# Kernel tuning notes

Hardware: AMD Instinct MI355X
Metric: run time of the kernel (lower is better)

The kernel has to match this reference:

```python
import jax, jax.numpy as jnp
import numpy as np

B, N, F, L = 4, 8192, 64, 2


def setup_inputs() -> dict:
    key = jax.random.key(0)
    k1, k2, k3 = jax.random.split(key, 3)
    x = jax.random.normal(k1, (B, N, F), dtype=jnp.float32)
    net_params = jax.random.normal(k2, (L * F * F,), dtype=jnp.float32)
    A = jax.random.normal(k3, (N, N), dtype=jnp.float32)
    return {"x": x, "t": 0, "net_params": net_params, "A": A}


def reference(x, t, net_params, A):
    # weights: [L, F, F]
    weights = net_params.reshape(L, F, F)
    # x: [B, N, F] (original does x.view(-1, A.size(1), features))
    z = x.reshape(-1, A.shape[1], F)
    for i in range(L):
        # GCN_operation: Z_out = A @ Z @ W_i  (the nested vmm loops emulate exactly this)
        h = jnp.einsum('mn,bnf->bmf', A, z)          # [B, N, F]
        z = jnp.einsum('bmf,fg->bmg', h, weights[i])  # [B, N, F]
        z = jax.nn.relu(z)
    return z
```

## Files before the change

kernel.cpp:

```cpp
#include <hip/hip_runtime.h>
#include <stdint.h>


#define MK 8192

typedef float f32x4 __attribute__((ext_vector_type(4)));
typedef uint32_t u32x4 __attribute__((ext_vector_type(4)));
typedef uint32_t u32x2 __attribute__((ext_vector_type(2)));
typedef __bf16 bf16x8 __attribute__((ext_vector_type(8)));

__device__ inline uint16_t f2bf(float f) {
  uint32_t u = __builtin_bit_cast(uint32_t, f);
  u += 0x7fffu + ((u >> 16) & 1u);
  return (uint16_t)(u >> 16);
}
__device__ inline float bf2f(uint32_t lo16) {
  return __builtin_bit_cast(float, lo16 << 16);
}

#define GLD(src, dstbase)                                                                    \
  __builtin_amdgcn_global_load_lds((const __attribute__((address_space(1))) uint32_t*)(src), \
                                   (__attribute__((address_space(3))) uint32_t*)(dstbase),   \
                                   16, 0, 0)

__global__ __launch_bounds__(256) void zw0(const float* __restrict__ x,
                                           const float* __restrict__ net,
                                           uint16_t* __restrict__ Zt) {
  __shared__ float Wl[64 * 64];
  __shared__ float rows[64][65];
  const int b = blockIdx.y, n0 = blockIdx.x * 64, tid = threadIdx.x;
  for (int i = tid * 4; i < 4096; i += 1024) {
    f32x4 v = *(const f32x4*)(net + i);
    Wl[i] = v[0]; Wl[i + 1] = v[1]; Wl[i + 2] = v[2]; Wl[i + 3] = v[3];
  }
  const float* src = x + ((uint64_t)b * MK + n0) * 64;
  for (int i = tid * 4; i < 4096; i += 1024) {
    f32x4 v = *(const f32x4*)(src + i);
    int r = i >> 6, f = i & 63;
    rows[r][f] = v[0]; rows[r][f + 1] = v[1]; rows[r][f + 2] = v[2]; rows[r][f + 3] = v[3];
  }
  __syncthreads();
  const int nl = tid & 63, g0 = (tid >> 6) * 16;
  float s[16];
#pragma unroll
  for (int j = 0; j < 16; ++j) s[j] = 0.f;
  for (int f = 0; f < 64; ++f) {
    float rv = rows[nl][f];
#pragma unroll
    for (int j = 0; j < 16; ++j) s[j] = fmaf(rv, Wl[f * 64 + g0 + j], s[j]);
  }
  uint16_t* dst = Zt + (uint64_t)(b * 64 + g0) * MK + n0 + nl;
#pragma unroll
  for (int j = 0; j < 16; ++j) dst[(uint64_t)j * MK] = f2bf(s[j]);
}

__global__ __launch_bounds__(512, 2) void gemm1(const float* __restrict__ Af,
                                                const uint16_t* __restrict__ Bt,
                                                uint16_t* __restrict__ Ab,
                                                uint16_t* __restrict__ P) {
  __shared__ __align__(16) uint16_t As[2][16384];
  __shared__ __align__(16) uint16_t Bs[2][16384];
  const int bid = (int)blockIdx.x;
  const int s = bid & 7, bm = bid >> 3;
  const int row0 = bm * 256, k0 = s * 1024;
  const int tid = threadIdx.x, wid = tid >> 6, lane = tid & 63;
  const int wr = wid >> 2, wc = wid & 3;

  const int lsub = lane >> 3;
  const int ksrc = ((lane & 7) ^ lsub) << 3;
  const uint16_t* gB0 = Bt + (uint64_t)(4 * wid * 8 + lsub) * MK + k0 + ksrc;
  const int lBo = 4 * wid * 512;

  const int arow = (8 * wid) * 4 + (lane >> 4);
  const int acol = (lane & 15) * 4;
  const float* gA0 = Af + (uint64_t)(row0 + arow) * MK + k0 + acol;
  const int koct = (lane & 15) >> 1, krem = (lane & 1) * 4;

  f32x4 acc[8][4] = {};
  f32x4 rv[8];

  auto loadA = [&](int kofs) {
#pragma unroll
    for (int j = 0; j < 8; ++j)
      rv[j] = __builtin_nontemporal_load((const f32x4*)(gA0 + (uint64_t)j * 4 * MK + kofs));
  };
  auto stageA = [&](int buf, int kofs) {
#pragma unroll
    for (int j = 0; j < 8; ++j) {
      const int r = arow + j * 4;
      u32x2 w;
      w[0] = (uint32_t)f2bf(rv[j][0]) | ((uint32_t)f2bf(rv[j][1]) << 16);
      w[1] = (uint32_t)f2bf(rv[j][2]) | ((uint32_t)f2bf(rv[j][3]) << 16);
      *(u32x2*)&As[buf][r * 64 + ((koct ^ (r & 7)) << 3) + krem] = w;
      *(u32x2*)(Ab + (uint64_t)(row0 + r) * MK + k0 + kofs + acol) = w;
    }
  };

  loadA(0);
#pragma unroll
  for (int j = 0; j < 4; ++j) GLD(gB0 + (uint64_t)j * 8 * MK, &Bs[0][lBo + j * 512]);
  stageA(0, 0);
  __syncthreads();

  int buf = 0;
  for (int t = 0; t < 16; ++t) {
    const int nxt = (t + 1) * 64;
    if (t < 15) {
      loadA(nxt);
#pragma unroll
      for (int j = 0; j < 4; ++j) GLD(gB0 + (uint64_t)j * 8 * MK + nxt, &Bs[buf ^ 1][lBo + j * 512]);
    }
#pragma unroll
    for (int kk = 0; kk < 2; ++kk) {
      const int kb = kk * 4 + (lane >> 4);
      bf16x8 a[8], b[4];
#pragma unroll
      for (int mi = 0; mi < 8; ++mi) {
        const int r = wr * 128 + mi * 16 + (lane & 15);
        a[mi] = *(const bf16x8*)&As[buf][r * 64 + ((kb ^ (r & 7)) << 3)];
      }
#pragma unroll
      for (int n = 0; n < 4; ++n) {
        const int r = wc * 64 + n * 16 + (lane & 15);
        b[n] = *(const bf16x8*)&Bs[buf][r * 64 + ((kb ^ (r & 7)) << 3)];
      }
#pragma unroll
      for (int mi = 0; mi < 8; ++mi)
#pragma unroll
        for (int n = 0; n < 4; ++n)
          acc[mi][n] = __builtin_amdgcn_mfma_f32_16x16x32_bf16(a[mi], b[n], acc[mi][n], 0, 0, 0);
    }
    if (t < 15) stageA(buf ^ 1, nxt);
    __syncthreads();
    buf ^= 1;
  }

  uint16_t* Pp = P + (uint64_t)s * 2097152;
  const int lr = (lane >> 4) * 4, lc = lane & 15;
#pragma unroll
  for (int mi = 0; mi < 8; ++mi)
#pragma unroll
    for (int n = 0; n < 4; ++n) {
      const int gr = row0 + wr * 128 + mi * 16 + lr;
      const int gc = wc * 64 + n * 16 + lc;
#pragma unroll
      for (int j = 0; j < 4; ++j)
        Pp[(uint64_t)(gr + j) * 256 + gc] = f2bf(acc[mi][n][j]);
    }
}

__global__ __launch_bounds__(512, 2) void gemm2(const uint16_t* __restrict__ Ab,
                                                const uint16_t* __restrict__ Bt,
                                                uint16_t* __restrict__ P) {
  __shared__ __align__(16) uint16_t As[2][16384];
  __shared__ __align__(16) uint16_t Bs[2][16384];
  const int bid = (int)blockIdx.x;
  const int s = bid & 7, bm = bid >> 3;
  const int row0 = bm * 256, k0 = s * 1024;
  const int tid = threadIdx.x, wid = tid >> 6, lane = tid & 63;
  const int wr = wid >> 2, wc = wid & 3;

  const int lsub = lane >> 3;
  const int ksrc = ((lane & 7) ^ lsub) << 3;
  const uint16_t* gA0 = Ab + (uint64_t)(row0 + 4 * wid * 8 + lsub) * MK + k0 + ksrc;
  const uint16_t* gB0 = Bt + (uint64_t)(4 * wid * 8 + lsub) * MK + k0 + ksrc;
  const int lo = 4 * wid * 512;

  f32x4 acc[8][4] = {};

#pragma unroll
  for (int j = 0; j < 4; ++j) {
    GLD(gA0 + (uint64_t)j * 8 * MK, &As[0][lo + j * 512]);
    GLD(gB0 + (uint64_t)j * 8 * MK, &Bs[0][lo + j * 512]);
  }

  int buf = 0;
  for (int t = 0; t < 16; ++t) {
    const int tko = ((t + 1) < 16 ? (t + 1) : 15) * 64;
#pragma unroll
    for (int j = 0; j < 4; ++j) {
      GLD(gA0 + (uint64_t)j * 8 * MK + tko, &As[buf ^ 1][lo + j * 512]);
      GLD(gB0 + (uint64_t)j * 8 * MK + tko, &Bs[buf ^ 1][lo + j * 512]);
    }
    asm volatile("s_waitcnt vmcnt(8)" ::: "memory");
    __builtin_amdgcn_s_barrier();
    __builtin_amdgcn_sched_barrier(0);

    bf16x8 b[4][2];
#pragma unroll
    for (int n = 0; n < 4; ++n)
#pragma unroll
      for (int kk = 0; kk < 2; ++kk) {
        const int r = wc * 64 + n * 16 + (lane & 15);
        const int kb = kk * 4 + (lane >> 4);
        b[n][kk] = *(const bf16x8*)&Bs[buf][r * 64 + ((kb ^ (r & 7)) << 3)];
      }
#pragma unroll
    for (int q = 0; q < 4; ++q) {
      bf16x8 a[2][2];
#pragma unroll
      for (int i = 0; i < 2; ++i)
#pragma unroll
        for (int kk = 0; kk < 2; ++kk) {
          const int r = wr * 128 + (2 * q + i) * 16 + (lane & 15);
          const int kb = kk * 4 + (lane >> 4);
          a[i][kk] = *(const bf16x8*)&As[buf][r * 64 + ((kb ^ (r & 7)) << 3)];
        }
      __builtin_amdgcn_s_setprio(1);
#pragma unroll
      for (int kk = 0; kk < 2; ++kk)
#pragma unroll
        for (int i = 0; i < 2; ++i)
#pragma unroll
          for (int n = 0; n < 4; ++n)
            acc[2 * q + i][n] =
                __builtin_amdgcn_mfma_f32_16x16x32_bf16(a[i][kk], b[n][kk], acc[2 * q + i][n], 0, 0, 0);
      __builtin_amdgcn_s_setprio(0);
      __builtin_amdgcn_sched_barrier(0);
    }
    __builtin_amdgcn_s_barrier();
    buf ^= 1;
  }

  uint16_t* Pp = P + (uint64_t)s * 2097152;
  const int lr = (lane >> 4) * 4, lc = lane & 15;
#pragma unroll
  for (int mi = 0; mi < 8; ++mi)
#pragma unroll
    for (int n = 0; n < 4; ++n) {
      const int gr = row0 + wr * 128 + mi * 16 + lr;
      const int gc = wc * 64 + n * 16 + lc;
#pragma unroll
      for (int j = 0; j < 4; ++j)
        Pp[(uint64_t)(gr + j) * 256 + gc] = f2bf(acc[mi][n][j]);
    }
}

__global__ __launch_bounds__(256) void zw1P(const uint16_t* __restrict__ P,
                                            const float* __restrict__ net,
                                            uint16_t* __restrict__ Zt) {
  __shared__ float Wl[64 * 64];
  __shared__ float rows[64][65];
  const int b = blockIdx.y, n0 = blockIdx.x * 64, tid = threadIdx.x;
  const float* Wsrc = net + 4096;
  for (int i = tid * 4; i < 4096; i += 1024) {
    f32x4 v = *(const f32x4*)(Wsrc + i);
    Wl[i] = v[0]; Wl[i + 1] = v[1]; Wl[i + 2] = v[2]; Wl[i + 3] = v[3];
  }
#pragma unroll
  for (int g = 0; g < 2; ++g) {
    const int idx = (tid + g * 256) * 8;
    const int r = idx >> 6, f0 = idx & 63;
    const uint16_t* base = P + (uint64_t)(n0 + r) * 256 + b * 64 + f0;
    float acc8[8] = {};
#pragma unroll
    for (int sp = 0; sp < 8; ++sp) {
      u32x4 v = *(const u32x4*)(base + (uint64_t)sp * 2097152);
#pragma unroll
      for (int j = 0; j < 4; ++j) {
        acc8[2 * j]     += bf2f(v[j] & 0xffffu);
        acc8[2 * j + 1] += bf2f(v[j] >> 16);
      }
    }
#pragma unroll
    for (int j = 0; j < 8; ++j) rows[r][f0 + j] = fmaxf(acc8[j], 0.0f);
  }
  __syncthreads();
  const int nl = tid & 63, g0 = (tid >> 6) * 16;
  float s[16];
#pragma unroll
  for (int j = 0; j < 16; ++j) s[j] = 0.f;
  for (int f = 0; f < 64; ++f) {
    float rv = rows[nl][f];
#pragma unroll
    for (int j = 0; j < 16; ++j) s[j] = fmaf(rv, Wl[f * 64 + g0 + j], s[j]);
  }
  uint16_t* dst = Zt + (uint64_t)(b * 64 + g0) * MK + n0 + nl;
#pragma unroll
  for (int j = 0; j < 16; ++j) dst[(uint64_t)j * MK] = f2bf(s[j]);
}

__global__ __launch_bounds__(256) void combineF(const uint16_t* __restrict__ P,
                                                float* __restrict__ out) {
  const uint64_t e = ((uint64_t)blockIdx.x * 256 + threadIdx.x) * 8;
  float acc8[8] = {};
#pragma unroll
  for (int sp = 0; sp < 8; ++sp) {
    u32x4 v = *(const u32x4*)&P[(uint64_t)sp * 2097152 + e];
#pragma unroll
    for (int j = 0; j < 4; ++j) {
      acc8[2 * j]     += bf2f(v[j] & 0xffffu);
      acc8[2 * j + 1] += bf2f(v[j] >> 16);
    }
  }
  const int m = (int)(e >> 8);
  const int c = (int)(e & 255);
  float* dst = &out[(((uint64_t)(c >> 6)) * MK + m) * 64 + (c & 63)];
  f32x4 w0, w1;
#pragma unroll
  for (int j = 0; j < 4; ++j) { w0[j] = fmaxf(acc8[j], 0.0f); w1[j] = fmaxf(acc8[4 + j], 0.0f); }
  *(f32x4*)dst = w0;
  *(f32x4*)(dst + 4) = w1;
}

extern "C" void kernel_launch(void* const* d_in, const int* in_sizes, int n_in,
                              void* d_out, int out_size, void* d_ws, size_t ws_size,
                              hipStream_t stream) {
  const float* x   = (const float*)d_in[0];
  const float* net = (const float*)d_in[2];
  const float* A   = (const float*)d_in[3];
  float* out = (float*)d_out;

  uint16_t* Ab = (uint16_t*)d_ws;
  uint16_t* Zt = (uint16_t*)((char*)d_ws + 134217728ull);
  uint16_t* P  = (uint16_t*)((char*)d_ws + 142606336ull);

  zw0<<<dim3(128, 4), dim3(256), 0, stream>>>(x, net, Zt);
  gemm1<<<dim3(256), dim3(512), 0, stream>>>(A, Zt, Ab, P);
  zw1P<<<dim3(128, 4), dim3(256), 0, stream>>>(P, net, Zt);
  gemm2<<<dim3(256), dim3(512), 0, stream>>>(Ab, Zt, P);
  combineF<<<dim3(1024), dim3(256), 0, stream>>>(P, out);
}
```

Measured before the change: 172.0 us.

## Shrink GEMM tiles to 64-row, 32-wide K steps with 1024 blocks

Both split-K GEMMs now use 64-row blocks of 256 threads, where each wave owns a 64x64 output tile, and K advances in 32-element steps instead of 256-row blocks with 64-element steps. The grid grows from 256 to 1024 blocks so the CUs are filled more evenly, and LDS per block shrinks so several blocks can share a CU. In exchange, each B tile is reused across fewer A rows, which raises global and L2 traffic for the Zt operand. The loops also drop the XOR swizzle, the explicit vmcnt/setprio scheduling in gemm2, and the wider MFMA batching, which can bring LDS bank conflicts and more barriers per unit of work.

```diff
diff --git a/kernel.cpp b/kernel.cpp
--- a/kernel.cpp
+++ b/kernel.cpp
@@ -54,83 +54,72 @@
   for (int j = 0; j < 16; ++j) dst[(uint64_t)j * MK] = f2bf(s[j]);
 }
 
-__global__ __launch_bounds__(512, 2) void gemm1(const float* __restrict__ Af,
+__global__ __launch_bounds__(256, 3) void gemm1(const float* __restrict__ Af,
                                                 const uint16_t* __restrict__ Bt,
                                                 uint16_t* __restrict__ Ab,
                                                 uint16_t* __restrict__ P) {
-  __shared__ __align__(16) uint16_t As[2][16384];
-  __shared__ __align__(16) uint16_t Bs[2][16384];
+  __shared__ __align__(16) uint16_t As[2][2048];
+  __shared__ __align__(16) uint16_t Bs[2][8192];
   const int bid = (int)blockIdx.x;
   const int s = bid & 7, bm = bid >> 3;
-  const int row0 = bm * 256, k0 = s * 1024;
+  const int row0 = bm * 64, k0 = s * 1024;
   const int tid = threadIdx.x, wid = tid >> 6, lane = tid & 63;
-  const int wr = wid >> 2, wc = wid & 3;
-
-  const int lsub = lane >> 3;
-  const int ksrc = ((lane & 7) ^ lsub) << 3;
-  const uint16_t* gB0 = Bt + (uint64_t)(4 * wid * 8 + lsub) * MK + k0 + ksrc;
-  const int lBo = 4 * wid * 512;
-
-  const int arow = (8 * wid) * 4 + (lane >> 4);
-  const int acol = (lane & 15) * 4;
-  const float* gA0 = Af + (uint64_t)(row0 + arow) * MK + k0 + acol;
-  const int koct = (lane & 15) >> 1, krem = (lane & 1) * 4;
-
-  f32x4 acc[8][4] = {};
-  f32x4 rv[8];
-
-  auto loadA = [&](int kofs) {
-#pragma unroll
-    for (int j = 0; j < 8; ++j)
-      rv[j] = __builtin_nontemporal_load((const f32x4*)(gA0 + (uint64_t)j * 4 * MK + kofs));
+
+  const int ar = tid >> 2, ao = (tid & 3) * 8;
+  const float* gA = Af + (uint64_t)(row0 + ar) * MK + k0 + ao;
+  uint16_t* AbW = Ab + (uint64_t)(row0 + ar) * MK + k0 + ao;
+
+  const int brow = lane >> 2, boct = (lane & 3) * 8;
+  const uint16_t* gB[4];
+#pragma unroll
+  for (int j = 0; j < 4; ++j)
+    gB[j] = Bt + (uint64_t)((4 * wid + j) * 16 + brow) * MK + k0 + boct;
+  const int lB = 4 * wid * 512;
+
+  f32x4 acc[4][4] = {};
+  f32x4 rv0, rv1;
+
+  auto loadA = [&](int kt) {
+    rv0 = __builtin_nontemporal_load((const f32x4*)(gA + kt));
+    rv1 = __builtin_nontemporal_load((const f32x4*)(gA + kt + 4));
   };
-  auto stageA = [&](int buf, int kofs) {
-#pragma unroll
-    for (int j = 0; j < 8; ++j) {
-      const int r = arow + j * 4;
-      u32x2 w;
-      w[0] = (uint32_t)f2bf(rv[j][0]) | ((uint32_t)f2bf(rv[j][1]) << 16);
-      w[1] = (uint32_t)f2bf(rv[j][2]) | ((uint32_t)f2bf(rv[j][3]) << 16);
-      *(u32x2*)&As[buf][r * 64 + ((koct ^ (r & 7)) << 3) + krem] = w;
-      *(u32x2*)(Ab + (uint64_t)(row0 + r) * MK + k0 + kofs + acol) = w;
-    }
+  auto stageA = [&](int buf, int kt) {
+    u32x4 w;
+    w[0] = (uint32_t)f2bf(rv0[0]) | ((uint32_t)f2bf(rv0[1]) << 16);
+    w[1] = (uint32_t)f2bf(rv0[2]) | ((uint32_t)f2bf(rv0[3]) << 16);
+    w[2] = (uint32_t)f2bf(rv1[0]) | ((uint32_t)f2bf(rv1[1]) << 16);
+    w[3] = (uint32_t)f2bf(rv1[2]) | ((uint32_t)f2bf(rv1[3]) << 16);
+    *(u32x4*)&As[buf][ar * 32 + ao] = w;
+    *(u32x4*)(AbW + kt) = w;
   };
 
   loadA(0);
-#pragma unroll
-  for (int j = 0; j < 4; ++j) GLD(gB0 + (uint64_t)j * 8 * MK, &Bs[0][lBo + j * 512]);
   stageA(0, 0);
+#pragma unroll
+  for (int j = 0; j < 4; ++j) GLD(gB[j], &Bs[0][lB + j * 512]);
   __syncthreads();
 
   int buf = 0;
-  for (int t = 0; t < 16; ++t) {
-    const int nxt = (t + 1) * 64;
-    if (t < 15) {
+  for (int t = 0; t < 32; ++t) {
+    const int nxt = (t + 1) * 32;
+    if (t < 31) {
       loadA(nxt);
 #pragma unroll
-      for (int j = 0; j < 4; ++j) GLD(gB0 + (uint64_t)j * 8 * MK + nxt, &Bs[buf ^ 1][lBo + j * 512]);
-    }
-#pragma unroll
-    for (int kk = 0; kk < 2; ++kk) {
-      const int kb = kk * 4 + (lane >> 4);
-      bf16x8 a[8], b[4];
-#pragma unroll
-      for (int mi = 0; mi < 8; ++mi) {
-        const int r = wr * 128 + mi * 16 + (lane & 15);
-        a[mi] = *(const bf16x8*)&As[buf][r * 64 + ((kb ^ (r & 7)) << 3)];
-      }
-#pragma unroll
-      for (int n = 0; n < 4; ++n) {
-        const int r = wc * 64 + n * 16 + (lane & 15);
-        b[n] = *(const bf16x8*)&Bs[buf][r * 64 + ((kb ^ (r & 7)) << 3)];
-      }
-#pragma unroll
-      for (int mi = 0; mi < 8; ++mi)
-#pragma unroll
-        for (int n = 0; n < 4; ++n)
-          acc[mi][n] = __builtin_amdgcn_mfma_f32_16x16x32_bf16(a[mi], b[n], acc[mi][n], 0, 0, 0);
-    }
-    if (t < 15) stageA(buf ^ 1, nxt);
+      for (int j = 0; j < 4; ++j) GLD(gB[j] + nxt, &Bs[buf ^ 1][lB + j * 512]);
+    }
+    bf16x8 a[4], b[4];
+#pragma unroll
+    for (int m = 0; m < 4; ++m)
+      a[m] = *(const bf16x8*)&As[buf][(m * 16 + (lane & 15)) * 32 + (lane >> 4) * 8];
+#pragma unroll
+    for (int n = 0; n < 4; ++n)
+      b[n] = *(const bf16x8*)&Bs[buf][(wid * 64 + n * 16 + (lane & 15)) * 32 + (lane >> 4) * 8];
+#pragma unroll
+    for (int m = 0; m < 4; ++m)
+#pragma unroll
+      for (int n = 0; n < 4; ++n)
+        acc[m][n] = __builtin_amdgcn_mfma_f32_16x16x32_bf16(a[m], b[n], acc[m][n], 0, 0, 0);
+    if (t < 31) stageA(buf ^ 1, nxt);
     __syncthreads();
     buf ^= 1;
   }
@@ -138,101 +127,77 @@
   uint16_t* Pp = P + (uint64_t)s * 2097152;
   const int lr = (lane >> 4) * 4, lc = lane & 15;
 #pragma unroll
-  for (int mi = 0; mi < 8; ++mi)
+  for (int m = 0; m < 4; ++m)
 #pragma unroll
     for (int n = 0; n < 4; ++n) {
-      const int gr = row0 + wr * 128 + mi * 16 + lr;
-      const int gc = wc * 64 + n * 16 + lc;
+      const int gr = row0 + m * 16 + lr;
+      const int gc = wid * 64 + n * 16 + lc;
 #pragma unroll
       for (int j = 0; j < 4; ++j)
-        Pp[(uint64_t)(gr + j) * 256 + gc] = f2bf(acc[mi][n][j]);
-    }
-}
-
-__global__ __launch_bounds__(512, 2) void gemm2(const uint16_t* __restrict__ Ab,
+        Pp[(uint64_t)(gr + j) * 256 + gc] = f2bf(acc[m][n][j]);
+    }
+}
+
+__global__ __launch_bounds__(256, 3) void gemm2(const uint16_t* __restrict__ Ab,
                                                 const uint16_t* __restrict__ Bt,
                                                 uint16_t* __restrict__ P) {
-  __shared__ __align__(16) uint16_t As[2][16384];
-  __shared__ __align__(16) uint16_t Bs[2][16384];
+  __shared__ __align__(16) uint16_t As[2][2048];
+  __shared__ __align__(16) uint16_t Bs[2][8192];
   const int bid = (int)blockIdx.x;
   const int s = bid & 7, bm = bid >> 3;
-  const int row0 = bm * 256, k0 = s * 1024;
+  const int row0 = bm * 64, k0 = s * 1024;
   const int tid = threadIdx.x, wid = tid >> 6, lane = tid & 63;
-  const int wr = wid >> 2, wc = wid & 3;
-
-  const int lsub = lane >> 3;
-  const int ksrc = ((lane & 7) ^ lsub) << 3;
-  const uint16_t* gA0 = Ab + (uint64_t)(row0 + 4 * wid * 8 + lsub) * MK + k0 + ksrc;
-  const uint16_t* gB0 = Bt + (uint64_t)(4 * wid * 8 + lsub) * MK + k0 + ksrc;
-  const int lo = 4 * wid * 512;
-
-  f32x4 acc[8][4] = {};
-
-#pragma unroll
-  for (int j = 0; j < 4; ++j) {
-    GLD(gA0 + (uint64_t)j * 8 * MK, &As[0][lo + j * 512]);
-    GLD(gB0 + (uint64_t)j * 8 * MK, &Bs[0][lo + j * 512]);
-  }
+
+  const int crow = lane >> 2, coct = (lane & 3) * 8;
+  const uint16_t* gA = Ab + (uint64_t)(row0 + wid * 16 + crow) * MK + k0 + coct;
+  const uint16_t* gB[4];
+#pragma unroll
+  for (int j = 0; j < 4; ++j)
+    gB[j] = Bt + (uint64_t)((4 * wid + j) * 16 + crow) * MK + k0 + coct;
+  const int lA = wid * 512, lB = 4 * wid * 512;
+
+  f32x4 acc[4][4] = {};
+
+  GLD(gA, &As[0][lA]);
+#pragma unroll
+  for (int j = 0; j < 4; ++j) GLD(gB[j], &Bs[0][lB + j * 512]);
+  __syncthreads();
 
   int buf = 0;
-  for (int t = 0; t < 16; ++t) {
-    const int tko = ((t + 1) < 16 ? (t + 1) : 15) * 64;
-#pragma unroll
-    for (int j = 0; j < 4; ++j) {
-      GLD(gA0 + (uint64_t)j * 8 * MK + tko, &As[buf ^ 1][lo + j * 512]);
-      GLD(gB0 + (uint64_t)j * 8 * MK + tko, &Bs[buf ^ 1][lo + j * 512]);
-    }
-    asm volatile("s_waitcnt vmcnt(8)" ::: "memory");
-    __builtin_amdgcn_s_barrier();
-    __builtin_amdgcn_sched_barrier(0);
-
-    bf16x8 b[4][2];
+  for (int t = 0; t < 32; ++t) {
+    if (t < 31) {
+      const int nxt = (t + 1) * 32;
+      GLD(gA + nxt, &As[buf ^ 1][lA]);
+#pragma unroll
+      for (int j = 0; j < 4; ++j) GLD(gB[j] + nxt, &Bs[buf ^ 1][lB + j * 512]);
+    }
+    bf16x8 a[4], b[4];
+#pragma unroll
+    for (int m = 0; m < 4; ++m)
+      a[m] = *(const bf16x8*)&As[buf][(m * 16 + (lane & 15)) * 32 + (lane >> 4) * 8];
 #pragma unroll
     for (int n = 0; n < 4; ++n)
-#pragma unroll
-      for (int kk = 0; kk < 2; ++kk) {
-        const int r = wc * 64 + n * 16 + (lane & 15);
-        const int kb = kk * 4 + (lane >> 4);
-        b[n][kk] = *(const bf16x8*)&Bs[buf][r * 64 + ((kb ^ (r & 7)) << 3)];
-      }
-#pragma unroll
-    for (int q = 0; q < 4; ++q) {
-      bf16x8 a[2][2];
-#pragma unroll
-      for (int i = 0; i < 2; ++i)
-#pragma unroll
-        for (int kk = 0; kk < 2; ++kk) {
-          const int r = wr * 128 + (2 * q + i) * 16 + (lane & 15);
-          const int kb = kk * 4 + (lane >> 4);
-          a[i][kk] = *(const bf16x8*)&As[buf][r * 64 + ((kb ^ (r & 7)) << 3)];
-        }
-      __builtin_amdgcn_s_setprio(1);
-#pragma unroll
-      for (int kk = 0; kk < 2; ++kk)
-#pragma unroll
-        for (int i = 0; i < 2; ++i)
-#pragma unroll
-          for (int n = 0; n < 4; ++n)
-            acc[2 * q + i][n] =
-                __builtin_amdgcn_mfma_f32_16x16x32_bf16(a[i][kk], b[n][kk], acc[2 * q + i][n], 0, 0, 0);
-      __builtin_amdgcn_s_setprio(0);
-      __builtin_amdgcn_sched_barrier(0);
-    }
-    __builtin_amdgcn_s_barrier();
+      b[n] = *(const bf16x8*)&Bs[buf][(wid * 64 + n * 16 + (lane & 15)) * 32 + (lane >> 4) * 8];
+#pragma unroll
+    for (int m = 0; m < 4; ++m)
+#pragma unroll
+      for (int n = 0; n < 4; ++n)
+        acc[m][n] = __builtin_amdgcn_mfma_f32_16x16x32_bf16(a[m], b[n], acc[m][n], 0, 0, 0);
+    __syncthreads();
     buf ^= 1;
   }
 
   uint16_t* Pp = P + (uint64_t)s * 2097152;
   const int lr = (lane >> 4) * 4, lc = lane & 15;
 #pragma unroll
-  for (int mi = 0; mi < 8; ++mi)
+  for (int m = 0; m < 4; ++m)
 #pragma unroll
     for (int n = 0; n < 4; ++n) {
-      const int gr = row0 + wr * 128 + mi * 16 + lr;
-      const int gc = wc * 64 + n * 16 + lc;
+      const int gr = row0 + m * 16 + lr;
+      const int gc = wid * 64 + n * 16 + lc;
 #pragma unroll
       for (int j = 0; j < 4; ++j)
-        Pp[(uint64_t)(gr + j) * 256 + gc] = f2bf(acc[mi][n][j]);
+        Pp[(uint64_t)(gr + j) * 256 + gc] = f2bf(acc[m][n][j]);
     }
 }
 
@@ -316,8 +281,8 @@
   uint16_t* P  = (uint16_t*)((char*)d_ws + 142606336ull);
 
   zw0<<<dim3(128, 4), dim3(256), 0, stream>>>(x, net, Zt);
-  gemm1<<<dim3(256), dim3(512), 0, stream>>>(A, Zt, Ab, P);
+  gemm1<<<dim3(1024), dim3(256), 0, stream>>>(A, Zt, Ab, P);
   zw1P<<<dim3(128, 4), dim3(256), 0, stream>>>(P, net, Zt);
-  gemm2<<<dim3(256), dim3(512), 0, stream>>>(Ab, Zt, P);
+  gemm2<<<dim3(1024), dim3(256), 0, stream>>>(Ab, Zt, P);
   combineF<<<dim3(1024), dim3(256), 0, stream>>>(P, out);
 }
```

New measurement: 236.0 us. +37.2%, slower.

## Shrink gemm2 tile to 128 rows with K-step 32 and double grid

Applied to the files above, without the earlier changes.

Reworks the second GEMM to use 128-row output tiles and a 32-wide K step instead of 256 rows and 64-wide K, and doubles the grid to 512 blocks. LDS use drops and more blocks are in flight, aiming for better occupancy and fewer idle compute units. In exchange it removes the XOR swizzle (so LDS bank conflicts are likely), the explicit vmcnt pipelining and setprio tricks, and uses full __syncthreads each iteration. The B tile is also reloaded twice as often relative to the compute done.

```diff
diff --git a/kernel.cpp b/kernel.cpp
--- a/kernel.cpp
+++ b/kernel.cpp
@@ -152,87 +152,62 @@
 __global__ __launch_bounds__(512, 2) void gemm2(const uint16_t* __restrict__ Ab,
                                                 const uint16_t* __restrict__ Bt,
                                                 uint16_t* __restrict__ P) {
-  __shared__ __align__(16) uint16_t As[2][16384];
-  __shared__ __align__(16) uint16_t Bs[2][16384];
+  __shared__ __align__(16) uint16_t As[2][4096];
+  __shared__ __align__(16) uint16_t Bs[2][8192];
   const int bid = (int)blockIdx.x;
   const int s = bid & 7, bm = bid >> 3;
-  const int row0 = bm * 256, k0 = s * 1024;
+  const int row0 = bm * 128, k0 = s * 1024;
   const int tid = threadIdx.x, wid = tid >> 6, lane = tid & 63;
   const int wr = wid >> 2, wc = wid & 3;
 
-  const int lsub = lane >> 3;
-  const int ksrc = ((lane & 7) ^ lsub) << 3;
-  const uint16_t* gA0 = Ab + (uint64_t)(row0 + 4 * wid * 8 + lsub) * MK + k0 + ksrc;
-  const uint16_t* gB0 = Bt + (uint64_t)(4 * wid * 8 + lsub) * MK + k0 + ksrc;
-  const int lo = 4 * wid * 512;
-
-  f32x4 acc[8][4] = {};
-
-#pragma unroll
-  for (int j = 0; j < 4; ++j) {
-    GLD(gA0 + (uint64_t)j * 8 * MK, &As[0][lo + j * 512]);
-    GLD(gB0 + (uint64_t)j * 8 * MK, &Bs[0][lo + j * 512]);
-  }
+  const int crow = lane >> 2, coct = (lane & 3) * 8;
+  const uint16_t* gA = Ab + (uint64_t)(row0 + wid * 16 + crow) * MK + k0 + coct;
+  const uint16_t* gB0 = Bt + (uint64_t)(wid * 16 + crow) * MK + k0 + coct;
+  const uint16_t* gB1 = Bt + (uint64_t)(128 + wid * 16 + crow) * MK + k0 + coct;
+  const int lA = wid * 512, lB0 = wid * 512, lB1 = 4096 + wid * 512;
+
+  f32x4 acc[4][4] = {};
+
+  GLD(gA, &As[0][lA]);
+  GLD(gB0, &Bs[0][lB0]);
+  GLD(gB1, &Bs[0][lB1]);
+  __syncthreads();
 
   int buf = 0;
-  for (int t = 0; t < 16; ++t) {
-    const int tko = ((t + 1) < 16 ? (t + 1) : 15) * 64;
-#pragma unroll
-    for (int j = 0; j < 4; ++j) {
-      GLD(gA0 + (uint64_t)j * 8 * MK + tko, &As[buf ^ 1][lo + j * 512]);
-      GLD(gB0 + (uint64_t)j * 8 * MK + tko, &Bs[buf ^ 1][lo + j * 512]);
-    }
-    asm volatile("s_waitcnt vmcnt(8)" ::: "memory");
-    __builtin_amdgcn_s_barrier();
-    __builtin_amdgcn_sched_barrier(0);
-
-    bf16x8 b[4][2];
+  for (int t = 0; t < 32; ++t) {
+    if (t < 31) {
+      const int nxt = (t + 1) * 32;
+      GLD(gA + nxt, &As[buf ^ 1][lA]);
+      GLD(gB0 + nxt, &Bs[buf ^ 1][lB0]);
+      GLD(gB1 + nxt, &Bs[buf ^ 1][lB1]);
+    }
+    bf16x8 a[4], b[4];
+#pragma unroll
+    for (int m = 0; m < 4; ++m)
+      a[m] = *(const bf16x8*)&As[buf][(wr * 64 + m * 16 + (lane & 15)) * 32 + (lane >> 4) * 8];
 #pragma unroll
     for (int n = 0; n < 4; ++n)
-#pragma unroll
-      for (int kk = 0; kk < 2; ++kk) {
-        const int r = wc * 64 + n * 16 + (lane & 15);
-        const int kb = kk * 4 + (lane >> 4);
-        b[n][kk] = *(const bf16x8*)&Bs[buf][r * 64 + ((kb ^ (r & 7)) << 3)];
-      }
-#pragma unroll
-    for (int q = 0; q < 4; ++q) {
-      bf16x8 a[2][2];
-#pragma unroll
-      for (int i = 0; i < 2; ++i)
-#pragma unroll
-        for (int kk = 0; kk < 2; ++kk) {
-          const int r = wr * 128 + (2 * q + i) * 16 + (lane & 15);
-          const int kb = kk * 4 + (lane >> 4);
-          a[i][kk] = *(const bf16x8*)&As[buf][r * 64 + ((kb ^ (r & 7)) << 3)];
-        }
-      __builtin_amdgcn_s_setprio(1);
-#pragma unroll
-      for (int kk = 0; kk < 2; ++kk)
-#pragma unroll
-        for (int i = 0; i < 2; ++i)
-#pragma unroll
-          for (int n = 0; n < 4; ++n)
-            acc[2 * q + i][n] =
-                __builtin_amdgcn_mfma_f32_16x16x32_bf16(a[i][kk], b[n][kk], acc[2 * q + i][n], 0, 0, 0);
-      __builtin_amdgcn_s_setprio(0);
-      __builtin_amdgcn_sched_barrier(0);
-    }
-    __builtin_amdgcn_s_barrier();
+      b[n] = *(const bf16x8*)&Bs[buf][(wc * 64 + n * 16 + (lane & 15)) * 32 + (lane >> 4) * 8];
+#pragma unroll
+    for (int m = 0; m < 4; ++m)
+#pragma unroll
+      for (int n = 0; n < 4; ++n)
+        acc[m][n] = __builtin_amdgcn_mfma_f32_16x16x32_bf16(a[m], b[n], acc[m][n], 0, 0, 0);
+    __syncthreads();
     buf ^= 1;
   }
 
   uint16_t* Pp = P + (uint64_t)s * 2097152;
   const int lr = (lane >> 4) * 4, lc = lane & 15;
 #pragma unroll
-  for (int mi = 0; mi < 8; ++mi)
+  for (int m = 0; m < 4; ++m)
 #pragma unroll
     for (int n = 0; n < 4; ++n) {
-      const int gr = row0 + wr * 128 + mi * 16 + lr;
+      const int gr = row0 + wr * 64 + m * 16 + lr;
       const int gc = wc * 64 + n * 16 + lc;
 #pragma unroll
       for (int j = 0; j < 4; ++j)
-        Pp[(uint64_t)(gr + j) * 256 + gc] = f2bf(acc[mi][n][j]);
+        Pp[(uint64_t)(gr + j) * 256 + gc] = f2bf(acc[m][n][j]);
     }
 }
 
@@ -318,6 +293,6 @@
   zw0<<<dim3(128, 4), dim3(256), 0, stream>>>(x, net, Zt);
   gemm1<<<dim3(256), dim3(512), 0, stream>>>(A, Zt, Ab, P);
   zw1P<<<dim3(128, 4), dim3(256), 0, stream>>>(P, net, Zt);
-  gemm2<<<dim3(256), dim3(512), 0, stream>>>(Ab, Zt, P);
+  gemm2<<<dim3(512), dim3(512), 0, stream>>>(Ab, Zt, P);
   combineF<<<dim3(1024), dim3(256), 0, stream>>>(P, out);
 }
```

Result: slower. 178.5 us (+3.7%).

## Interleave half-tile global-to-LDS staging with per-quarter MFMA phases in gemm2

Applied to the files above, without the earlier changes.

Restructures the gemm2 main loop into an 8-phase software pipeline. Each phase issues a half-tile of A or B global-to-LDS loads, reads one quarter of the A fragments from LDS, and then runs 16 MFMAs, with barriers and lgkmcnt/vmcnt waits placed per phase. The aim is to spread memory issue evenly across the compute and overlap it with MFMA work, instead of issuing all loads at the top of each k-step. The trade-off is many more barriers per iteration and fragile hand-tuned waitcnt counts.

```diff
diff --git a/kernel.cpp b/kernel.cpp
--- a/kernel.cpp
+++ b/kernel.cpp
@@ -22,6 +22,12 @@
   __builtin_amdgcn_global_load_lds((const __attribute__((address_space(1))) uint32_t*)(src), \
                                    (__attribute__((address_space(3))) uint32_t*)(dstbase),   \
                                    16, 0, 0)
+#define BAR __builtin_amdgcn_s_barrier()
+#define LGKM0                                          \
+  do {                                                 \
+    asm volatile("s_waitcnt lgkmcnt(0)" ::: "memory"); \
+    __builtin_amdgcn_sched_barrier(0);                 \
+  } while (0)
 
 __global__ __launch_bounds__(256) void zw0(const float* __restrict__ x,
                                            const float* __restrict__ net,
@@ -152,74 +158,109 @@
 __global__ __launch_bounds__(512, 2) void gemm2(const uint16_t* __restrict__ Ab,
                                                 const uint16_t* __restrict__ Bt,
                                                 uint16_t* __restrict__ P) {
-  __shared__ __align__(16) uint16_t As[2][16384];
-  __shared__ __align__(16) uint16_t Bs[2][16384];
+  __shared__ __align__(16) uint16_t AL[2][16384];
+  __shared__ __align__(16) uint16_t BL[2][16384];
   const int bid = (int)blockIdx.x;
   const int s = bid & 7, bm = bid >> 3;
   const int row0 = bm * 256, k0 = s * 1024;
   const int tid = threadIdx.x, wid = tid >> 6, lane = tid & 63;
   const int wr = wid >> 2, wc = wid & 3;
 
-  const int lsub = lane >> 3;
-  const int ksrc = ((lane & 7) ^ lsub) << 3;
-  const uint16_t* gA0 = Ab + (uint64_t)(row0 + 4 * wid * 8 + lsub) * MK + k0 + ksrc;
-  const uint16_t* gB0 = Bt + (uint64_t)(4 * wid * 8 + lsub) * MK + k0 + ksrc;
-  const int lo = 4 * wid * 512;
+  const int kst = ((lane & 7) ^ (lane >> 3)) << 3;
+  const int srow = lane >> 3;
+  const int fr = lane & 15, fk = lane >> 4;
 
   f32x4 acc[8][4] = {};
 
-#pragma unroll
-  for (int j = 0; j < 4; ++j) {
-    GLD(gA0 + (uint64_t)j * 8 * MK, &As[0][lo + j * 512]);
-    GLD(gB0 + (uint64_t)j * 8 * MK, &Bs[0][lo + j * 512]);
-  }
-
-  int buf = 0;
-  for (int t = 0; t < 16; ++t) {
-    const int tko = ((t + 1) < 16 ? (t + 1) : 15) * 64;
-#pragma unroll
-    for (int j = 0; j < 4; ++j) {
-      GLD(gA0 + (uint64_t)j * 8 * MK + tko, &As[buf ^ 1][lo + j * 512]);
-      GLD(gB0 + (uint64_t)j * 8 * MK + tko, &Bs[buf ^ 1][lo + j * 512]);
-    }
-    asm volatile("s_waitcnt vmcnt(8)" ::: "memory");
-    __builtin_amdgcn_s_barrier();
-    __builtin_amdgcn_sched_barrier(0);
-
-    bf16x8 b[4][2];
+  auto stgA = [&](int bi, int half, int t) {
+#pragma unroll
+    for (int e = 0; e < 2; ++e) {
+      const int c = 2 * wid + e;
+      GLD(Ab + (uint64_t)(row0 + half * 128 + c * 8 + srow) * MK + k0 + t * 64 + kst,
+          &AL[bi][half * 8192 + c * 512]);
+    }
+  };
+  auto stgB = [&](int bi, int half, int t) {
+#pragma unroll
+    for (int e = 0; e < 2; ++e) {
+      const int c = 2 * wid + e;
+      GLD(Bt + (uint64_t)(half * 128 + c * 8 + srow) * MK + k0 + t * 64 + kst,
+          &BL[bi][half * 8192 + c * 512]);
+    }
+  };
+
+  bf16x8 b[4][2], a[2][2];
+  auto rdB = [&](int bi) {
+    const uint16_t* L = bi ? BL[1] : BL[0];
 #pragma unroll
     for (int n = 0; n < 4; ++n)
 #pragma unroll
       for (int kk = 0; kk < 2; ++kk) {
-        const int r = wc * 64 + n * 16 + (lane & 15);
-        const int kb = kk * 4 + (lane >> 4);
-        b[n][kk] = *(const bf16x8*)&Bs[buf][r * 64 + ((kb ^ (r & 7)) << 3)];
-      }
-#pragma unroll
-    for (int q = 0; q < 4; ++q) {
-      bf16x8 a[2][2];
+        const int r = wc * 64 + n * 16 + fr;
+        b[n][kk] = *(const bf16x8*)&L[r * 64 + (((kk * 4 + fk) ^ (r & 7)) << 3)];
+      }
+  };
+  auto rdA = [&](int bi, int q) {
+    const uint16_t* L = bi ? AL[1] : AL[0];
+#pragma unroll
+    for (int i = 0; i < 2; ++i)
+#pragma unroll
+      for (int kk = 0; kk < 2; ++kk) {
+        const int r = wr * 128 + (2 * q + i) * 16 + fr;
+        a[i][kk] = *(const bf16x8*)&L[r * 64 + (((kk * 4 + fk) ^ (r & 7)) << 3)];
+      }
+  };
+  auto mfma16 = [&](int q) {
+    __builtin_amdgcn_s_setprio(1);
+#pragma unroll
+    for (int kk = 0; kk < 2; ++kk)
 #pragma unroll
       for (int i = 0; i < 2; ++i)
 #pragma unroll
-        for (int kk = 0; kk < 2; ++kk) {
-          const int r = wr * 128 + (2 * q + i) * 16 + (lane & 15);
-          const int kb = kk * 4 + (lane >> 4);
-          a[i][kk] = *(const bf16x8*)&As[buf][r * 64 + ((kb ^ (r & 7)) << 3)];
-        }
-      __builtin_amdgcn_s_setprio(1);
-#pragma unroll
-      for (int kk = 0; kk < 2; ++kk)
-#pragma unroll
-        for (int i = 0; i < 2; ++i)
-#pragma unroll
-          for (int n = 0; n < 4; ++n)
-            acc[2 * q + i][n] =
-                __builtin_amdgcn_mfma_f32_16x16x32_bf16(a[i][kk], b[n][kk], acc[2 * q + i][n], 0, 0, 0);
-      __builtin_amdgcn_s_setprio(0);
-      __builtin_amdgcn_sched_barrier(0);
-    }
-    __builtin_amdgcn_s_barrier();
-    buf ^= 1;
+        for (int n = 0; n < 4; ++n)
+          acc[2 * q + i][n] =
+              __builtin_amdgcn_mfma_f32_16x16x32_bf16(a[i][kk], b[n][kk], acc[2 * q + i][n], 0, 0, 0);
+    __builtin_amdgcn_s_setprio(0);
+  };
+
+  stgA(0, 0, 0); stgA(0, 1, 0);
+  stgB(0, 0, 0); stgB(0, 1, 0);
+  stgB(1, 0, 1); stgB(1, 1, 1);
+  asm volatile("s_waitcnt vmcnt(4)" ::: "memory");
+  BAR;
+
+  for (int j = 0; j < 8; ++j) {
+    const int t1 = 2 * j + 1;
+    const int t2 = (2 * j + 2 < 16) ? 2 * j + 2 : 15;
+    const int t3 = (2 * j + 3 < 16) ? 2 * j + 3 : 15;
+
+    rdB(0); rdA(0, 0); stgA(1, 0, t1);
+    asm volatile("s_waitcnt lgkmcnt(8)" ::: "memory");
+    BAR; LGKM0; mfma16(0); BAR;
+
+    rdA(0, 1); stgA(1, 1, t1);
+    BAR; LGKM0; mfma16(1); BAR;
+
+    rdA(0, 2); stgB(0, 0, t2);
+    BAR; LGKM0; mfma16(2); BAR;
+
+    rdA(0, 3); stgB(0, 1, t2);
+    asm volatile("s_waitcnt vmcnt(4)" ::: "memory");
+    BAR; LGKM0; mfma16(3); BAR;
+
+    rdB(1); rdA(1, 0); stgA(0, 0, t2);
+    asm volatile("s_waitcnt lgkmcnt(8)" ::: "memory");
+    BAR; LGKM0; mfma16(0); BAR;
+
+    rdA(1, 1); stgA(0, 1, t2);
+    BAR; LGKM0; mfma16(1); BAR;
+
+    rdA(1, 2); stgB(1, 0, t3);
+    BAR; LGKM0; mfma16(2); BAR;
+
+    rdA(1, 3); stgB(1, 1, t3);
+    asm volatile("s_waitcnt vmcnt(4)" ::: "memory");
+    BAR; LGKM0; mfma16(3); BAR;
   }
 
   uint16_t* Pp = P + (uint64_t)s * 2097152;
```

After: 175.3 us. About the same (+1.9%).
